# Kernel optimization log

Measured on AMD Instinct MI355X. Metric: run time of the kernel, lower is better.

Reference implementation:

```python
import jax, jax.numpy as jnp
import numpy as np

D_MODEL = 768
NUM_HEADS = 12
D_K = D_MODEL // NUM_HEADS
B, S = 8, 1024


def setup_inputs() -> dict:
    key = jax.random.key(0)
    ks = jax.random.split(key, 10)
    sc = 1.0 / np.sqrt(D_MODEL)
    inp = {
        'x': jax.random.normal(ks[0], (B, S, D_MODEL), dtype=jnp.float32),
        'mask': jnp.tril(jnp.ones((1, 1, S, S), dtype=jnp.int32)),
        'W_q': jax.random.normal(ks[1], (D_MODEL, D_MODEL), jnp.float32) * sc,
        'b_q': jnp.zeros((D_MODEL,), jnp.float32),
        'W_k': jax.random.normal(ks[2], (D_MODEL, D_MODEL), jnp.float32) * sc,
        'b_k': jnp.zeros((D_MODEL,), jnp.float32),
        'W_v': jax.random.normal(ks[3], (D_MODEL, D_MODEL), jnp.float32) * sc,
        'b_v': jnp.zeros((D_MODEL,), jnp.float32),
        'W_o': jax.random.normal(ks[4], (D_MODEL, D_MODEL), jnp.float32) * sc,
        'b_o': jnp.zeros((D_MODEL,), jnp.float32),
    }
    return inp


def reference(x, mask, W_q, b_q, W_k, b_k, W_v, b_v, W_o, b_o):
    b, s, d = x.shape
    # project (torch Linear: y = x @ W.T + b; here weights stored as [in, out])
    q = (x @ W_q + b_q).reshape(b, s, NUM_HEADS, D_K).transpose(0, 2, 1, 3)
    k = (x @ W_k + b_k).reshape(b, s, NUM_HEADS, D_K).transpose(0, 2, 1, 3)
    v = (x @ W_v + b_v).reshape(b, s, NUM_HEADS, D_K).transpose(0, 2, 1, 3)
    scores = jnp.einsum('bhqd,bhkd->bhqk', q, k) / jnp.sqrt(jnp.float32(D_K))
    scores = jnp.where(mask == 0, jnp.float32(-jnp.inf), scores)
    attn = jax.nn.softmax(scores, axis=-1)  # dropout: eval mode (identity)
    out = jnp.einsum('bhqk,bhkd->bhqd', attn, v)
    out = out.transpose(0, 2, 1, 3).reshape(b, s, d)
    return out @ W_o + b_o
```

## Files before the change

kernel.cpp:

```cpp
#include <hip/hip_runtime.h>
#include <hip/hip_bf16.h>
#include <stdint.h>

typedef __attribute__((ext_vector_type(8))) short short8;
typedef __attribute__((ext_vector_type(4))) short s16x4;
typedef __attribute__((ext_vector_type(4))) float f32x4;

#define GLDS16(gp, lp) __builtin_amdgcn_global_load_lds( \
    (const __attribute__((address_space(1))) void*)(gp), \
    (__attribute__((address_space(3))) void*)(lp), 16, 0, 0)

__device__ __forceinline__ unsigned short f2bf(float f) {
  union { float f; unsigned u; } v; v.f = f;
  unsigned r = v.u + 0x7FFFu + ((v.u >> 16) & 1u);
  return (unsigned short)(r >> 16);
}

__device__ __forceinline__ short bfpack(float f) {
  union { float f; unsigned u; } v; v.f = f;
  return (short)((v.u + 0x8000u) >> 16);
}

__global__ __launch_bounds__(256) void cast_x(const float* __restrict__ x,
                                              unsigned short* __restrict__ o, int n4) {
  int i = blockIdx.x * 256 + threadIdx.x;
  if (i < n4) {
    float4 v = ((const float4*)x)[i];
    union { unsigned short u[4]; unsigned long long ll; } r;
    r.u[0] = f2bf(v.x); r.u[1] = f2bf(v.y); r.u[2] = f2bf(v.z); r.u[3] = f2bf(v.w);
    ((unsigned long long*)o)[i] = r.ll;
  }
}

__global__ __launch_bounds__(256) void cast_wt4(const float* __restrict__ W0,
                                                const float* __restrict__ W1,
                                                const float* __restrict__ W2,
                                                const float* __restrict__ W3,
                                                unsigned short* __restrict__ T0,
                                                unsigned short* __restrict__ T1,
                                                unsigned short* __restrict__ T2,
                                                unsigned short* __restrict__ T3) {
  __shared__ float t[16][17];
  const int z = blockIdx.z;
  const float* W = z == 0 ? W0 : (z == 1 ? W1 : (z == 2 ? W2 : W3));
  unsigned short* Wt = z == 0 ? T0 : (z == 1 ? T1 : (z == 2 ? T2 : T3));
  int tx = threadIdx.x, ty = threadIdx.y;
  int c0 = blockIdx.x * 16, r0 = blockIdx.y * 16;
  t[ty][tx] = W[(size_t)(r0 + ty) * 768 + c0 + tx];
  __syncthreads();
  Wt[(size_t)(c0 + ty) * 768 + r0 + tx] = f2bf(t[tx][ty]);
}

__device__ __forceinline__ void gemm_core(const unsigned short* __restrict__ A,
                                          const unsigned short* __restrict__ Bt,
                                          int row0, int col0, f32x4 acc[4][4],
                                          unsigned short* sA, unsigned short* sB) {
  const int t = threadIdx.x, l = t & 63;
  const int w = t >> 6, wr = w >> 1, wc = w & 1;
  const int lr = l & 15, lk = l >> 4;
  const int rs = t >> 2;
  const int csw = ((t & 3) ^ (rs & 3) ^ ((t >> 4) & 3)) * 8;
  const int rsw = (lr & 3) ^ (lr >> 2);
  const unsigned short* Ar = A + (size_t)(row0 + rs) * 768 + csw;
  const unsigned short* Br = Bt + (size_t)(col0 + rs) * 768 + csw;

#define GSTAGE(BUF, K0)                                                     \
  do {                                                                      \
    GLDS16(Ar + (K0), sA + (BUF) * 4096 + t * 8);                           \
    GLDS16(Ar + (size_t)64 * 768 + (K0), sA + (BUF) * 4096 + 2048 + t * 8); \
    GLDS16(Br + (K0), sB + (BUF) * 4096 + t * 8);                           \
    GLDS16(Br + (size_t)64 * 768 + (K0), sB + (BUF) * 4096 + 2048 + t * 8); \
  } while (0)

#define GCOMPUTE(PAR)                                                            \
  do {                                                                           \
    const unsigned short* cA = sA + (PAR) * 4096;                                \
    const unsigned short* cB = sB + (PAR) * 4096;                                \
    short8 af[4], bfr[4];                                                        \
    _Pragma("unroll") for (int i = 0; i < 4; ++i)                                \
        af[i] = *(const short8*)(cA + (wr * 64 + i * 16 + lr) * 32 + ((lk ^ rsw) * 8)); \
    _Pragma("unroll") for (int i = 0; i < 4; ++i)                                \
        bfr[i] = *(const short8*)(cB + (wc * 64 + i * 16 + lr) * 32 + ((lk ^ rsw) * 8)); \
    __builtin_amdgcn_s_setprio(1);                                               \
    _Pragma("unroll") for (int i = 0; i < 4; ++i)                                \
        _Pragma("unroll") for (int j = 0; j < 4; ++j)                            \
            acc[i][j] = __builtin_amdgcn_mfma_f32_16x16x32_bf16(af[i], bfr[j], acc[i][j], 0, 0, 0); \
    __builtin_amdgcn_s_setprio(0);                                               \
  } while (0)

  GSTAGE(0, 0);
  GSTAGE(1, 32);
#pragma unroll 1
  for (int kt = 0; kt < 22; ++kt) {
    asm volatile("s_waitcnt vmcnt(4)" ::: "memory");
    __builtin_amdgcn_s_barrier();
    __builtin_amdgcn_sched_barrier(0);
    GCOMPUTE(kt & 1);
    __builtin_amdgcn_sched_barrier(0);
    __builtin_amdgcn_s_barrier();
    __builtin_amdgcn_sched_barrier(0);
    GSTAGE(kt & 1, (kt + 2) * 32);
  }
  asm volatile("s_waitcnt vmcnt(4)" ::: "memory");
  __builtin_amdgcn_s_barrier();
  __builtin_amdgcn_sched_barrier(0);
  GCOMPUTE(0);
  asm volatile("s_waitcnt vmcnt(0)" ::: "memory");
  __builtin_amdgcn_s_barrier();
  __builtin_amdgcn_sched_barrier(0);
  GCOMPUTE(1);
#undef GSTAGE
#undef GCOMPUTE
}

__global__ __launch_bounds__(256, 3) void gemm_qkv(const unsigned short* __restrict__ A,
                                                   const unsigned short* __restrict__ Bt,
                                                   const float* __restrict__ bq,
                                                   const float* __restrict__ bk,
                                                   const float* __restrict__ bv,
                                                   unsigned short* __restrict__ Qb,
                                                   unsigned short* __restrict__ Kb,
                                                   unsigned short* __restrict__ Vt) {
  __shared__ unsigned short sA[2][128 * 32];
  __shared__ unsigned short sB[2][128 * 32];
  const int row0 = blockIdx.x * 128, col0 = blockIdx.y * 128;
  f32x4 acc[4][4] = {};
  gemm_core(A, Bt, row0, col0, acc, &sA[0][0], &sB[0][0]);

  const int l = threadIdx.x & 63, w = threadIdx.x >> 6;
  const int wr = w >> 1, wc = w & 1, lr = l & 15, lk = l >> 4;
  const int which = (blockIdx.y * 128) / 768;
  const int ncb = col0 - which * 768;
  if (which == 2) {
    const int bb = row0 >> 10;
    const int sb = (row0 & 1023) + wr * 64;
#pragma unroll
    for (int i = 0; i < 4; ++i) {
      const int sp = sb + (i >> 1) * 32 + lk * 8 + (i & 1) * 4;
#pragma unroll
      for (int j = 0; j < 4; ++j) {
        const int n = ncb + wc * 64 + j * 16 + lr;
        const float bn = bv[n];
        s16x4 vv;
#pragma unroll
        for (int r = 0; r < 4; ++r) vv[r] = (short)f2bf(acc[i][j][r] + bn);
        *(s16x4*)(Vt + ((size_t)(bb * 768 + n)) * 1024 + sp) = vv;
      }
    }
  } else {
    unsigned short* outp = which == 0 ? Qb : Kb;
    const float* bias = which == 0 ? bq : bk;
    const float scale = which == 0 ? 0.18033688011112042f : 1.0f;
#pragma unroll
    for (int i = 0; i < 4; ++i)
#pragma unroll
      for (int j = 0; j < 4; ++j) {
        int n = ncb + wc * 64 + j * 16 + lr;
        float bn = bias[n];
#pragma unroll
        for (int r = 0; r < 4; ++r) {
          int m = row0 + wr * 64 + i * 16 + lk * 4 + r;
          outp[(size_t)m * 768 + n] = f2bf((acc[i][j][r] + bn) * scale);
        }
      }
  }
}

__global__ __launch_bounds__(256, 3) void gemm_out(const unsigned short* __restrict__ A,
                                                   const unsigned short* __restrict__ Bt,
                                                   const float* __restrict__ bias,
                                                   float* __restrict__ C) {
  __shared__ unsigned short sA[2][128 * 32];
  __shared__ unsigned short sB[2][128 * 32];
  const int row0 = blockIdx.x * 128, col0 = blockIdx.y * 128;
  f32x4 acc[4][4] = {};
  gemm_core(A, Bt, row0, col0, acc, &sA[0][0], &sB[0][0]);

  const int l = threadIdx.x & 63, w = threadIdx.x >> 6;
  const int wr = w >> 1, wc = w & 1, lr = l & 15, lk = l >> 4;
#pragma unroll
  for (int i = 0; i < 4; ++i)
#pragma unroll
    for (int j = 0; j < 4; ++j) {
      int n = col0 + wc * 64 + j * 16 + lr;
      float bn = bias[n];
#pragma unroll
      for (int r = 0; r < 4; ++r) {
        int m = row0 + wr * 64 + i * 16 + lk * 4 + r;
        C[(size_t)m * 768 + n] = acc[i][j][r] + bn;
      }
    }
}

__global__ __launch_bounds__(256, 3) void attn(const unsigned short* __restrict__ Q,
                                               const unsigned short* __restrict__ Kg,
                                               const unsigned short* __restrict__ V2,
                                               unsigned short* __restrict__ O) {
  __shared__ unsigned short Kl[2][4096];
  __shared__ unsigned short Vl[2][4096];
  const int tid = threadIdx.x;
  const int l = tid & 63, w = tid >> 6;
  const int lr = l & 15, lk = l >> 4;
  const int o = blockIdx.x;
  const int b = o & 7, rem = o >> 3, pair = rem & 7, h = rem >> 3;
  const int hd = h * 64;
  const size_t bS = (size_t)b * 1024;
  const unsigned short* Kbase = Kg + bS * 768 + hd;
  const unsigned short* Vbase = V2 + ((size_t)b * 768 + hd) * 1024;
  const int rs = tid >> 3;
  const int kcol = ((tid & 7) ^ (rs & 7)) * 8;
  const int swz = (lr & 7);
  const int qloc = w * 16 + lr;

#define STAGE(BUF, T)                                                          \
  do {                                                                         \
    const size_t kv0_ = (size_t)(T) * 64;                                      \
    GLDS16(Kbase + (kv0_ + rs) * 768 + kcol, &Kl[BUF][tid * 8]);               \
    GLDS16(Kbase + (kv0_ + rs + 32) * 768 + kcol, &Kl[BUF][(256 + tid) * 8]);  \
    GLDS16(Vbase + (size_t)rs * 1024 + kv0_ + kcol, &Vl[BUF][tid * 8]);        \
    GLDS16(Vbase + (size_t)(rs + 32) * 1024 + kv0_ + kcol,                     \
           &Vl[BUF][(256 + tid) * 8]);                                         \
  } while (0)

#pragma unroll 1
  for (int half = 0; half < 2; ++half) {
    const int qt = half ? 15 - pair : pair;
    const int qw = qt * 64 + w * 16;
    const int ntile = qt + 1;
    short8 bq0, bq1;
    {
      size_t qb = (bS + qw + lr) * 768 + hd + lk * 8;
      bq0 = *(const short8*)(Q + qb);
      bq1 = *(const short8*)(Q + qb + 32);
    }
    f32x4 oc0 = {}, oc1 = {}, oc2 = {}, oc3 = {};
    float lsum = 0.f;

    __syncthreads();
    STAGE(0, 0);

#pragma unroll 1
    for (int t = 0; t < ntile; ++t) {
      __syncthreads();
      if (t + 1 < ntile) STAGE((t + 1) & 1, t + 1);
      const unsigned short* Kb_ = Kl[t & 1];
      const unsigned short* Vb_ = Vl[t & 1];
      short8 kf00 = *(const short8*)(Kb_ + (0 * 16 + lr) * 64 + (((0 * 4 + lk) ^ swz) * 8));
      short8 kf01 = *(const short8*)(Kb_ + (0 * 16 + lr) * 64 + (((1 * 4 + lk) ^ swz) * 8));
      short8 kf10 = *(const short8*)(Kb_ + (1 * 16 + lr) * 64 + (((0 * 4 + lk) ^ swz) * 8));
      short8 kf11 = *(const short8*)(Kb_ + (1 * 16 + lr) * 64 + (((1 * 4 + lk) ^ swz) * 8));
      short8 kf20 = *(const short8*)(Kb_ + (2 * 16 + lr) * 64 + (((0 * 4 + lk) ^ swz) * 8));
      short8 kf21 = *(const short8*)(Kb_ + (2 * 16 + lr) * 64 + (((1 * 4 + lk) ^ swz) * 8));
      short8 kf30 = *(const short8*)(Kb_ + (3 * 16 + lr) * 64 + (((0 * 4 + lk) ^ swz) * 8));
      short8 kf31 = *(const short8*)(Kb_ + (3 * 16 + lr) * 64 + (((1 * 4 + lk) ^ swz) * 8));
      short8 vf00 = *(const short8*)(Vb_ + (0 * 16 + lr) * 64 + (((0 * 4 + lk) ^ swz) * 8));
      short8 vf01 = *(const short8*)(Vb_ + (0 * 16 + lr) * 64 + (((1 * 4 + lk) ^ swz) * 8));
      short8 vf10 = *(const short8*)(Vb_ + (1 * 16 + lr) * 64 + (((0 * 4 + lk) ^ swz) * 8));
      short8 vf11 = *(const short8*)(Vb_ + (1 * 16 + lr) * 64 + (((1 * 4 + lk) ^ swz) * 8));
      short8 vf20 = *(const short8*)(Vb_ + (2 * 16 + lr) * 64 + (((0 * 4 + lk) ^ swz) * 8));
      short8 vf21 = *(const short8*)(Vb_ + (2 * 16 + lr) * 64 + (((1 * 4 + lk) ^ swz) * 8));
      short8 vf30 = *(const short8*)(Vb_ + (3 * 16 + lr) * 64 + (((0 * 4 + lk) ^ swz) * 8));
      short8 vf31 = *(const short8*)(Vb_ + (3 * 16 + lr) * 64 + (((1 * 4 + lk) ^ swz) * 8));

      f32x4 s0 = {}, s1 = {}, s2 = {}, s3 = {};
      __builtin_amdgcn_s_setprio(1);
      s0 = __builtin_amdgcn_mfma_f32_16x16x32_bf16(kf00, bq0, s0, 0, 0, 0);
      s0 = __builtin_amdgcn_mfma_f32_16x16x32_bf16(kf01, bq1, s0, 0, 0, 0);
      s1 = __builtin_amdgcn_mfma_f32_16x16x32_bf16(kf10, bq0, s1, 0, 0, 0);
      s1 = __builtin_amdgcn_mfma_f32_16x16x32_bf16(kf11, bq1, s1, 0, 0, 0);
      s2 = __builtin_amdgcn_mfma_f32_16x16x32_bf16(kf20, bq0, s2, 0, 0, 0);
      s2 = __builtin_amdgcn_mfma_f32_16x16x32_bf16(kf21, bq1, s2, 0, 0, 0);
      s3 = __builtin_amdgcn_mfma_f32_16x16x32_bf16(kf30, bq0, s3, 0, 0, 0);
      s3 = __builtin_amdgcn_mfma_f32_16x16x32_bf16(kf31, bq1, s3, 0, 0, 0);
      __builtin_amdgcn_s_setprio(0);

      if (t == ntile - 1) {
        const int kb = lk * 4;
#pragma unroll
        for (int r = 0; r < 4; ++r) {
          if (kb + 0 + r > qloc) s0[r] = -1e30f;
          if (kb + 16 + r > qloc) s1[r] = -1e30f;
          if (kb + 32 + r > qloc) s2[r] = -1e30f;
          if (kb + 48 + r > qloc) s3[r] = -1e30f;
        }
      }
      float p0[4], p1[4], p2[4], p3[4];
#pragma unroll
      for (int r = 0; r < 4; ++r) {
        p0[r] = __builtin_amdgcn_exp2f(s0[r]);
        p1[r] = __builtin_amdgcn_exp2f(s1[r]);
        p2[r] = __builtin_amdgcn_exp2f(s2[r]);
        p3[r] = __builtin_amdgcn_exp2f(s3[r]);
      }
      lsum += ((p0[0] + p0[1]) + (p0[2] + p0[3])) + ((p1[0] + p1[1]) + (p1[2] + p1[3])) +
              ((p2[0] + p2[1]) + (p2[2] + p2[3])) + ((p3[0] + p3[1]) + (p3[2] + p3[3]));
      short8 pb0, pb1;
#pragma unroll
      for (int r = 0; r < 4; ++r) {
        pb0[r] = bfpack(p0[r]); pb0[r + 4] = bfpack(p1[r]);
        pb1[r] = bfpack(p2[r]); pb1[r + 4] = bfpack(p3[r]);
      }
      __builtin_amdgcn_s_setprio(1);
      oc0 = __builtin_amdgcn_mfma_f32_16x16x32_bf16(vf00, pb0, oc0, 0, 0, 0);
      oc0 = __builtin_amdgcn_mfma_f32_16x16x32_bf16(vf01, pb1, oc0, 0, 0, 0);
      oc1 = __builtin_amdgcn_mfma_f32_16x16x32_bf16(vf10, pb0, oc1, 0, 0, 0);
      oc1 = __builtin_amdgcn_mfma_f32_16x16x32_bf16(vf11, pb1, oc1, 0, 0, 0);
      oc2 = __builtin_amdgcn_mfma_f32_16x16x32_bf16(vf20, pb0, oc2, 0, 0, 0);
      oc2 = __builtin_amdgcn_mfma_f32_16x16x32_bf16(vf21, pb1, oc2, 0, 0, 0);
      oc3 = __builtin_amdgcn_mfma_f32_16x16x32_bf16(vf30, pb0, oc3, 0, 0, 0);
      oc3 = __builtin_amdgcn_mfma_f32_16x16x32_bf16(vf31, pb1, oc3, 0, 0, 0);
      __builtin_amdgcn_s_setprio(0);
    }

    lsum += __shfl_xor(lsum, 16);
    lsum += __shfl_xor(lsum, 32);
    const float inv = 1.f / lsum;
    unsigned short* op = O + (bS + qw + lr) * 768 + hd + lk * 4;
    s16x4 o0, o1, o2, o3;
#pragma unroll
    for (int r = 0; r < 4; ++r) {
      o0[r] = (short)f2bf(oc0[r] * inv);
      o1[r] = (short)f2bf(oc1[r] * inv);
      o2[r] = (short)f2bf(oc2[r] * inv);
      o3[r] = (short)f2bf(oc3[r] * inv);
    }
    *(s16x4*)(op) = o0;
    *(s16x4*)(op + 16) = o1;
    *(s16x4*)(op + 32) = o2;
    *(s16x4*)(op + 48) = o3;
  }
#undef STAGE
}

extern "C" void kernel_launch(void* const* d_in, const int* in_sizes, int n_in,
                              void* d_out, int out_size, void* d_ws, size_t ws_size,
                              hipStream_t stream) {
  const float* x  = (const float*)d_in[0];
  const float* Wq = (const float*)d_in[2]; const float* bq = (const float*)d_in[3];
  const float* Wk = (const float*)d_in[4]; const float* bk = (const float*)d_in[5];
  const float* Wv = (const float*)d_in[6]; const float* bv = (const float*)d_in[7];
  const float* Wo = (const float*)d_in[8]; const float* bo = (const float*)d_in[9];
  float* out = (float*)d_out;

  char* ws = (char*)d_ws;
  unsigned short* xb  = (unsigned short*)ws;
  unsigned short* WtQ = (unsigned short*)(ws + (size_t)12582912);
  unsigned short* WtK = WtQ + 589824;
  unsigned short* WtV = WtK + 589824;
  unsigned short* WtO = WtV + 589824;
  unsigned short* Qb  = (unsigned short*)(ws + (size_t)12582912 + (size_t)4 * 1179648);
  unsigned short* Kb  = Qb + 6291456;
  unsigned short* Vt  = Kb + 2 * 6291456;
  unsigned short* Ob  = xb;

  cast_x<<<6144, 256, 0, stream>>>(x, xb, 1572864);
  cast_wt4<<<dim3(48, 48, 4), dim3(16, 16), 0, stream>>>(Wq, Wk, Wv, Wo, WtQ, WtK, WtV, WtO);
  gemm_qkv<<<dim3(64, 18), 256, 0, stream>>>(xb, WtQ, bq, bk, bv, Qb, Kb, Vt);
  attn<<<768, 256, 0, stream>>>(Qb, Kb, Vt, Ob);
  gemm_out<<<dim3(64, 6), 256, 0, stream>>>(Ob, WtO, bo, out);
}
```

Before: 107.3 us.

## Triple-buffer LDS staging in GEMM and attention to drop second barrier

New measurement: 105.8 us. Within noise of the previous version (-1.4%).

```diff
diff --git a/kernel.cpp b/kernel.cpp
--- a/kernel.cpp
+++ b/kernel.cpp
@@ -72,10 +72,10 @@
     GLDS16(Br + (size_t)64 * 768 + (K0), sB + (BUF) * 4096 + 2048 + t * 8); \
   } while (0)
 
-#define GCOMPUTE(PAR)                                                            \
+#define GCOMPUTE(BUF)                                                            \
   do {                                                                           \
-    const unsigned short* cA = sA + (PAR) * 4096;                                \
-    const unsigned short* cB = sB + (PAR) * 4096;                                \
+    const unsigned short* cA = sA + (BUF) * 4096;                                \
+    const unsigned short* cB = sB + (BUF) * 4096;                                \
     short8 af[4], bfr[4];                                                        \
     _Pragma("unroll") for (int i = 0; i < 4; ++i)                                \
         af[i] = *(const short8*)(cA + (wr * 64 + i * 16 + lr) * 32 + ((lk ^ rsw) * 8)); \
@@ -90,25 +90,21 @@
 
   GSTAGE(0, 0);
   GSTAGE(1, 32);
+  int b0 = 0, b2 = 2;
 #pragma unroll 1
-  for (int kt = 0; kt < 22; ++kt) {
+  for (int kt = 0; kt < 23; ++kt) {
     asm volatile("s_waitcnt vmcnt(4)" ::: "memory");
     __builtin_amdgcn_s_barrier();
     __builtin_amdgcn_sched_barrier(0);
-    GCOMPUTE(kt & 1);
-    __builtin_amdgcn_sched_barrier(0);
-    __builtin_amdgcn_s_barrier();
-    __builtin_amdgcn_sched_barrier(0);
-    GSTAGE(kt & 1, (kt + 2) * 32);
+    if (kt < 22) GSTAGE(b2, (kt + 2) * 32);
+    GCOMPUTE(b0);
+    b0 = (b0 == 2) ? 0 : b0 + 1;
+    b2 = (b2 == 2) ? 0 : b2 + 1;
   }
-  asm volatile("s_waitcnt vmcnt(4)" ::: "memory");
-  __builtin_amdgcn_s_barrier();
-  __builtin_amdgcn_sched_barrier(0);
-  GCOMPUTE(0);
   asm volatile("s_waitcnt vmcnt(0)" ::: "memory");
   __builtin_amdgcn_s_barrier();
   __builtin_amdgcn_sched_barrier(0);
-  GCOMPUTE(1);
+  GCOMPUTE(b0);
 #undef GSTAGE
 #undef GCOMPUTE
 }
@@ -121,8 +117,8 @@
                                                    unsigned short* __restrict__ Qb,
                                                    unsigned short* __restrict__ Kb,
                                                    unsigned short* __restrict__ Vt) {
-  __shared__ unsigned short sA[2][128 * 32];
-  __shared__ unsigned short sB[2][128 * 32];
+  __shared__ unsigned short sA[3][4096];
+  __shared__ unsigned short sB[3][4096];
   const int row0 = blockIdx.x * 128, col0 = blockIdx.y * 128;
   f32x4 acc[4][4] = {};
   gemm_core(A, Bt, row0, col0, acc, &sA[0][0], &sB[0][0]);
@@ -170,8 +166,8 @@
                                                    const unsigned short* __restrict__ Bt,
                                                    const float* __restrict__ bias,
                                                    float* __restrict__ C) {
-  __shared__ unsigned short sA[2][128 * 32];
-  __shared__ unsigned short sB[2][128 * 32];
+  __shared__ unsigned short sA[3][4096];
+  __shared__ unsigned short sB[3][4096];
   const int row0 = blockIdx.x * 128, col0 = blockIdx.y * 128;
   f32x4 acc[4][4] = {};
   gemm_core(A, Bt, row0, col0, acc, &sA[0][0], &sB[0][0]);
@@ -196,8 +192,8 @@
                                                const unsigned short* __restrict__ Kg,
                                                const unsigned short* __restrict__ V2,
                                                unsigned short* __restrict__ O) {
-  __shared__ unsigned short Kl[2][4096];
-  __shared__ unsigned short Vl[2][4096];
+  __shared__ unsigned short Kl[3][4096];
+  __shared__ unsigned short Vl[3][4096];
   const int tid = threadIdx.x;
   const int l = tid & 63, w = tid >> 6;
   const int lr = l & 15, lk = l >> 4;
@@ -227,6 +223,7 @@
     const int qt = half ? 15 - pair : pair;
     const int qw = qt * 64 + w * 16;
     const int ntile = qt + 1;
+    __syncthreads();
     short8 bq0, bq1;
     {
       size_t qb = (bS + qw + lr) * 768 + hd + lk * 8;
@@ -236,15 +233,24 @@
     f32x4 oc0 = {}, oc1 = {}, oc2 = {}, oc3 = {};
     float lsum = 0.f;
 
-    __syncthreads();
     STAGE(0, 0);
+    if (ntile > 1) STAGE(1, 1);
+    int b0 = 0, b2 = 2;
 
 #pragma unroll 1
     for (int t = 0; t < ntile; ++t) {
-      __syncthreads();
-      if (t + 1 < ntile) STAGE((t + 1) & 1, t + 1);
-      const unsigned short* Kb_ = Kl[t & 1];
-      const unsigned short* Vb_ = Vl[t & 1];
+      if (t < ntile - 1) {
+        asm volatile("s_waitcnt vmcnt(4)" ::: "memory");
+      } else {
+        asm volatile("s_waitcnt vmcnt(0)" ::: "memory");
+      }
+      __builtin_amdgcn_s_barrier();
+      __builtin_amdgcn_sched_barrier(0);
+      if (t + 2 < ntile) STAGE(b2, t + 2);
+      const unsigned short* Kb_ = Kl[b0];
+      const unsigned short* Vb_ = Vl[b0];
+      b0 = (b0 == 2) ? 0 : b0 + 1;
+      b2 = (b2 == 2) ? 0 : b2 + 1;
       short8 kf00 = *(const short8*)(Kb_ + (0 * 16 + lr) * 64 + (((0 * 4 + lk) ^ swz) * 8));
       short8 kf01 = *(const short8*)(Kb_ + (0 * 16 + lr) * 64 + (((1 * 4 + lk) ^ swz) * 8));
       short8 kf10 = *(const short8*)(Kb_ + (1 * 16 + lr) * 64 + (((0 * 4 + lk) ^ swz) * 8));
```
